# Kernel tuning notes

Measured on AMD Instinct MI355X. Metric: run time of the kernel, lower is better.

Reference implementation:

```python
import jax, jax.numpy as jnp
import numpy as np

N, E = 50000, 800000
F_IN, H, C = 128, 4, 32
NEG_SLOPE = 0.2

def setup_inputs() -> dict:
    key = jax.random.key(0)
    k1, k2, k3, k4, k5, k6 = jax.random.split(key, 6)
    x = jax.random.normal(k1, (N, F_IN), dtype=jnp.float32)
    edge_index = jax.random.randint(k2, (2, E), 0, N, dtype=jnp.int64)
    # GATConv params: lin weight [F_IN, H*C], att_src/att_dst [H, C], bias [H*C]
    W = jax.random.normal(k3, (F_IN, H * C), dtype=jnp.float32) * (1.0 / np.sqrt(F_IN))
    att_src = jax.random.normal(k4, (H, C), dtype=jnp.float32) * (1.0 / np.sqrt(C))
    att_dst = jax.random.normal(k5, (H, C), dtype=jnp.float32) * (1.0 / np.sqrt(C))
    bias = jax.random.normal(k6, (H * C,), dtype=jnp.float32) * 0.01
    return {"x": x, "edge_index": edge_index, "W": W, "att_src": att_src, "att_dst": att_dst, "bias": bias}

def reference(x, edge_index, W, att_src, att_dst, bias):
    # Linear transform: [N, H, C]
    h = (x @ W).reshape(N, H, C)
    # Per-node attention logits: [N, H]
    a_src = jnp.einsum('nhc,hc->nh', h, att_src)
    a_dst = jnp.einsum('nhc,hc->nh', h, att_dst)
    # PyG GATConv adds self-loops by default
    loop = jnp.arange(N, dtype=edge_index.dtype)
    src = jnp.concatenate([edge_index[0], loop])  # message source j
    dst = jnp.concatenate([edge_index[1], loop])  # message target i
    # Edge logits + LeakyReLU: [E+N, H]
    e = jax.nn.leaky_relu(a_src[src] + a_dst[dst], NEG_SLOPE)
    # Segment softmax over incoming edges per target node
    m = jax.ops.segment_max(e, dst, num_segments=N)  # [N, H]
    e_exp = jnp.exp(e - m[dst])
    denom = jax.ops.segment_sum(e_exp, dst, num_segments=N)  # [N, H]
    att = e_exp / denom[dst]  # [E+N, H]
    # Scatter-add weighted messages: [N, H, C]
    out = jax.ops.segment_sum(h[src] * att[:, :, None], dst, num_segments=N)
    return out.reshape(N, H * C) + bias
```

## Files before the change

kernel.cpp:

```cpp
#include <hip/hip_runtime.h>
#include <cstdint>

#define NNODES 50000
#define NEDGES 800000
#define NEG 0.2f
#define NBKT 196
#define BCAP 5120
#define GEMM_BLOCKS 782

typedef __attribute__((ext_vector_type(8))) short short8;
typedef __attribute__((ext_vector_type(4))) float f32x4;

#define AS_STRIDE 136
#define CS_STRIDE 132

__device__ __forceinline__ float leaky(float v) { return v > 0.f ? v : NEG * v; }

__device__ __forceinline__ unsigned short f2bf(float f) {
    unsigned int u = __float_as_uint(f);
    u += 0x7fff + ((u >> 16) & 1);
    return (unsigned short)(u >> 16);
}

template <int NW>
__device__ __forceinline__ int block_excl_scan(int v, int t) {
    __shared__ int wsum[NW];
    const int lane = t & 63, wv = t >> 6;
    int x = v;
    #pragma unroll
    for (int m = 1; m < 64; m <<= 1) {
        int u = __shfl_up(x, m);
        if (lane >= m) x += u;
    }
    if (lane == 63) wsum[wv] = x;
    __syncthreads();
    if (t == 0) {
        int run = 0;
        #pragma unroll
        for (int i = 0; i < NW; ++i) { int tmp = wsum[i]; wsum[i] = run; run += tmp; }
    }
    __syncthreads();
    return x - v + wsum[wv];
}

__global__ __launch_bounds__(256) void wt_k(const float* __restrict__ W,
                                            const float* __restrict__ att_src,
                                            const float* __restrict__ att_dst,
                                            unsigned short* __restrict__ wt,
                                            uint4* __restrict__ battf,
                                            int* __restrict__ bcnt) {
    const int t = threadIdx.x;
    if (blockIdx.x < 16) {
        int i = blockIdx.x * 256 + t;
        int k = i >> 5, n4 = (i & 31) * 4;
        float4 wv = ((const float4*)W)[i];
        wt[(n4 + 0) * 128 + k] = f2bf(wv.x);
        wt[(n4 + 1) * 128 + k] = f2bf(wv.y);
        wt[(n4 + 2) * 128 + k] = f2bf(wv.z);
        wt[(n4 + 3) * 128 + k] = f2bf(wv.w);
        return;
    }
    __shared__ float wsd[2][128][4];
    if (t < NBKT) bcnt[t] = 0;
    const int k = t & 127, which = t >> 7;
    const float* av = which ? att_dst : att_src;
    #pragma unroll
    for (int h = 0; h < 4; ++h) {
        float s = 0.f;
        #pragma unroll
        for (int c4 = 0; c4 < 8; ++c4) {
            float4 wv = ((const float4*)(W + k * 128 + h * 32))[c4];
            float4 a  = ((const float4*)(av + h * 32))[c4];
            s += wv.x * a.x + wv.y * a.y + wv.z * a.z + wv.w * a.w;
        }
        wsd[which][k][h] = s;
    }
    __syncthreads();
    const int s = t >> 6, lane = t & 63;
    const int quad = lane >> 4, m16 = lane & 15;
    unsigned short fr[8];
    #pragma unroll
    for (int j = 0; j < 8; ++j) {
        int kk = s * 32 + quad * 8 + j;
        float v = 0.f;
        if (m16 < 4)      v = wsd[0][kk][m16];
        else if (m16 < 8) v = wsd[1][kk][m16 - 4];
        fr[j] = f2bf(v);
    }
    battf[s * 64 + lane] = make_uint4(
        ((unsigned)fr[1] << 16) | fr[0], ((unsigned)fr[3] << 16) | fr[2],
        ((unsigned)fr[5] << 16) | fr[4], ((unsigned)fr[7] << 16) | fr[6]);
}

__global__ __launch_bounds__(256) void fused_k(const float* __restrict__ x,
                                               const unsigned short* __restrict__ wt,
                                               const uint4* __restrict__ battf,
                                               unsigned short* __restrict__ hb,
                                               float* __restrict__ a_src,
                                               float* __restrict__ a_dst,
                                               const int* __restrict__ ei,
                                               int* __restrict__ bcnt,
                                               unsigned int* __restrict__ bktdata) {
    __shared__ __align__(16) char smem[52224];
    const int tid = threadIdx.x;

    if (blockIdx.x < GEMM_BLOCKS) {
        unsigned short* As = (unsigned short*)smem;
        unsigned short* Bs = (unsigned short*)(smem + 17408);
        float*          Cs = (float*)smem;
        const int rbase = blockIdx.x * 64;

        #pragma unroll
        for (int i = 0; i < 8; ++i) {
            int f = tid + i * 256;
            int r = f >> 5, c4 = (f & 31) * 4;
            float4 xv = make_float4(0.f, 0.f, 0.f, 0.f);
            if (rbase + r < NNODES) xv = ((const float4*)x)[(size_t)(rbase + r) * 32 + (f & 31)];
            unsigned int p0 = ((unsigned int)f2bf(xv.y) << 16) | f2bf(xv.x);
            unsigned int p1 = ((unsigned int)f2bf(xv.w) << 16) | f2bf(xv.z);
            *(uint2*)(As + r * AS_STRIDE + c4) = make_uint2(p0, p1);
        }
        #pragma unroll
        for (int i = 0; i < 8; ++i) {
            int c = tid + i * 256;
            int n = c >> 4, k8 = (c & 15) * 8;
            uint4 wv = ((const uint4*)wt)[c];
            *(uint4*)(Bs + n * AS_STRIDE + k8) = wv;
        }
        __syncthreads();

        const int lane = tid & 63, w = tid >> 6;
        const int quad = lane >> 4, m16 = lane & 15;

        short8 af[4];
        #pragma unroll
        for (int s = 0; s < 4; ++s)
            af[s] = *(const short8*)(As + (w * 16 + m16) * AS_STRIDE + s * 32 + quad * 8);

        f32x4 acc[8];
        #pragma unroll
        for (int t = 0; t < 8; ++t) acc[t] = (f32x4){0.f, 0.f, 0.f, 0.f};

        #pragma unroll
        for (int t = 0; t < 8; ++t) {
            #pragma unroll
            for (int s = 0; s < 4; ++s) {
                short8 bf = *(const short8*)(Bs + (t * 16 + m16) * AS_STRIDE + s * 32 + quad * 8);
                acc[t] = __builtin_amdgcn_mfma_f32_16x16x32_bf16(af[s], bf, acc[t], 0, 0, 0);
            }
        }

        f32x4 accL = (f32x4){0.f, 0.f, 0.f, 0.f};
        #pragma unroll
        for (int s = 0; s < 4; ++s) {
            uint4 bw = battf[s * 64 + lane];
            accL = __builtin_amdgcn_mfma_f32_16x16x32_bf16(af[s], *(short8*)&bw, accL, 0, 0, 0);
        }
        __syncthreads();

        #pragma unroll
        for (int t = 0; t < 8; ++t)
            #pragma unroll
            for (int r = 0; r < 4; ++r)
                Cs[(w * 16 + quad * 4 + r) * CS_STRIDE + t * 16 + m16] = acc[t][r];
        __syncthreads();

        const int cp = lane;
        #pragma unroll
        for (int r = 0; r < 16; ++r) {
            int row = w * 16 + r;
            int row_g = rbase + row;
            float2 cv = *(const float2*)(Cs + row * CS_STRIDE + 2 * cp);
            ushort2 hs;
            hs.x = f2bf(cv.x); hs.y = f2bf(cv.y);
            if (row_g < NNODES) ((ushort2*)(hb + (size_t)row_g * 128))[cp] = hs;
        }
        #pragma unroll
        for (int r = 0; r < 4; ++r) {
            int row_g = rbase + w * 16 + quad * 4 + r;
            if (row_g < NNODES) {
                if (m16 < 4)      a_src[row_g * 4 + m16]       = accL[r];
                else if (m16 < 8) a_dst[row_g * 4 + (m16 - 4)] = accL[r];
            }
        }
    } else {
        int* lhist = (int*)smem;
        int* lofs  = lhist + NBKT;
        int* lcur  = lofs + NBKT;
        int* gbase = lcur + NBKT;
        unsigned int* staged = (unsigned int*)(gbase + NBKT);
        const int b = blockIdx.x - GEMM_BLOCKS, t = tid;
        for (int i = t; i < NBKT; i += 256) lhist[i] = 0;
        __syncthreads();
        unsigned int pk[16];
        int bk[16];
        const int e0 = b * 4096;
        #pragma unroll
        for (int i = 0; i < 16; ++i) {
            int e = e0 + i * 256 + t;
            if (e < NEDGES) {
                int s = ei[e], d = ei[NEDGES + e];
                bk[i] = d >> 8;
                pk[i] = ((unsigned)bk[i] << 24) | ((unsigned)(d & 255) << 16) | (unsigned)s;
                atomicAdd(&lhist[bk[i]], 1);
            } else bk[i] = -1;
        }
        __syncthreads();
        int v = (t < NBKT) ? lhist[t] : 0;
        int excl = block_excl_scan<4>(v, t);
        if (t < NBKT) { lofs[t] = excl; lcur[t] = excl; }
        __syncthreads();
        if (t < NBKT) gbase[t] = (v > 0) ? atomicAdd(&bcnt[t], v) : 0;
        #pragma unroll
        for (int i = 0; i < 16; ++i) {
            if (bk[i] >= 0) {
                int pos = atomicAdd(&lcur[bk[i]], 1);
                staged[pos] = pk[i];
            }
        }
        __syncthreads();
        const int total = lofs[NBKT - 1] + lhist[NBKT - 1];
        for (int i = t; i < total; i += 256) {
            unsigned int ent = staged[i];
            int bb = ent >> 24;
            int pos = gbase[bb] + (i - lofs[bb]);
            bktdata[(size_t)bb * BCAP + pos] = ent & 0x00FFFFFFu;
        }
    }
}

__global__ __launch_bounds__(512) void sort_k(const int* __restrict__ bcnt,
                                              const unsigned int* __restrict__ bktdata,
                                              int* __restrict__ off,
                                              int* __restrict__ csr) {
    __shared__ unsigned int staged[BCAP];
    __shared__ int lcnt[256];
    __shared__ int lcur[256];
    __shared__ int sbase, scnt;
    const int b = blockIdx.x, t = threadIdx.x;
    int bv = (t < NBKT) ? bcnt[t] : 0;
    int bexcl = block_excl_scan<8>(bv, t);
    if (t == b) { sbase = bexcl; scnt = bv; }
    if (t < 256) lcnt[t] = 0;
    __syncthreads();
    const int cnt = scnt, base = sbase;
    for (int i = t; i < cnt; i += 512) staged[i] = bktdata[(size_t)b * BCAP + i];
    __syncthreads();
    for (int i = t; i < cnt; i += 512) atomicAdd(&lcnt[(staged[i] >> 16) & 0xFF], 1);
    __syncthreads();
    int v = (t < 256) ? lcnt[t] : 0;
    int excl = block_excl_scan<8>(v, t);
    if (t < 256) {
        lcur[t] = excl;
        const int node = b * 256 + t;
        if (node <= NNODES) off[node] = base + excl;
    }
    __syncthreads();
    for (int i = t; i < cnt; i += 512) {
        unsigned int ent = staged[i];
        int pos = atomicAdd(&lcur[(ent >> 16) & 0xFF], 1);
        csr[base + pos] = (int)(ent & 0xFFFFu);
    }
}

__global__ __launch_bounds__(256) void gather_k(const int* __restrict__ off,
                                                const int* __restrict__ csr,
                                                const unsigned short* __restrict__ hb,
                                                const float* __restrict__ a_src,
                                                const float* __restrict__ a_dst,
                                                const float* __restrict__ bias,
                                                float* __restrict__ out) {
    const int wid = threadIdx.x >> 6, lane = threadIdx.x & 63;
    const int n = blockIdx.x * 4 + wid;
    if (n >= NNODES) return;
    const int head = lane >> 4;
    const int sub  = lane & 15;
    const int g = head, q = sub;
    const int head_c = q >> 2;

    const float a_d = a_dst[n * 4 + head];
    float acc[8];
    #pragma unroll
    for (int k = 0; k < 8; ++k) acc[k] = 0.f;

    if (g == 0) {
        float wsc = __expf(leaky(a_src[n * 4 + head_c] + a_dst[n * 4 + head_c]));
        uint4 hv = ((const uint4*)(hb + (size_t)n * 128))[q];
        acc[0] = wsc * __uint_as_float(hv.x << 16);
        acc[1] = wsc * __uint_as_float(hv.x & 0xffff0000u);
        acc[2] = wsc * __uint_as_float(hv.y << 16);
        acc[3] = wsc * __uint_as_float(hv.y & 0xffff0000u);
        acc[4] = wsc * __uint_as_float(hv.z << 16);
        acc[5] = wsc * __uint_as_float(hv.z & 0xffff0000u);
        acc[6] = wsc * __uint_as_float(hv.w << 16);
        acc[7] = wsc * __uint_as_float(hv.w & 0xffff0000u);
    }
    float denom = (sub == 0) ? __expf(leaky(a_src[n * 4 + head] + a_d)) : 0.f;

    const int beg = off[n], end = off[n + 1];
    for (int base = beg; base < end; base += 16) {
        int m = end - base; if (m > 16) m = 16;
        int s = 0;
        float w = 0.f;
        if (sub < m) {
            s = csr[base + sub];
            w = __expf(leaky(a_src[s * 4 + head] + a_d));
        }
        denom += w;
        #pragma unroll
        for (int jj = 0; jj < 4; ++jj) {
            int j = jj * 4 + g;
            int   sj = __shfl(s, j);
            float wj = __shfl(w, (head_c << 4) | j);
            if (j < m) {
                uint4 hv = ((const uint4*)(hb + (size_t)sj * 128))[q];
                acc[0] += wj * __uint_as_float(hv.x << 16);
                acc[1] += wj * __uint_as_float(hv.x & 0xffff0000u);
                acc[2] += wj * __uint_as_float(hv.y << 16);
                acc[3] += wj * __uint_as_float(hv.y & 0xffff0000u);
                acc[4] += wj * __uint_as_float(hv.z << 16);
                acc[5] += wj * __uint_as_float(hv.z & 0xffff0000u);
                acc[6] += wj * __uint_as_float(hv.w << 16);
                acc[7] += wj * __uint_as_float(hv.w & 0xffff0000u);
            }
        }
    }
    #pragma unroll
    for (int mm = 8; mm >= 1; mm >>= 1) denom += __shfl_xor(denom, mm, 16);
    const float inv = __frcp_rn(__shfl(denom, head_c << 4));
    #pragma unroll
    for (int k = 0; k < 8; ++k) {
        acc[k] += __shfl_xor(acc[k], 16);
        acc[k] += __shfl_xor(acc[k], 32);
    }
    if (g == 0) {
        float4 b0 = ((const float4*)bias)[2 * q];
        float4 b1 = ((const float4*)bias)[2 * q + 1];
        float4* orow = (float4*)(out + (size_t)n * 128);
        orow[2 * q]     = make_float4(acc[0] * inv + b0.x, acc[1] * inv + b0.y,
                                      acc[2] * inv + b0.z, acc[3] * inv + b0.w);
        orow[2 * q + 1] = make_float4(acc[4] * inv + b1.x, acc[5] * inv + b1.y,
                                      acc[6] * inv + b1.z, acc[7] * inv + b1.w);
    }
}

extern "C" void kernel_launch(void* const* d_in, const int* in_sizes, int n_in,
                              void* d_out, int out_size, void* d_ws, size_t ws_size,
                              hipStream_t stream) {
    const float* x     = (const float*)d_in[0];
    const int*   ei    = (const int*)d_in[1];
    const float* W     = (const float*)d_in[2];
    const float* att_s = (const float*)d_in[3];
    const float* att_d = (const float*)d_in[4];
    const float* bias  = (const float*)d_in[5];
    float*       out   = (float*)d_out;
    char*        ws    = (char*)d_ws;

    unsigned short* hb = (unsigned short*)(ws);
    float* a_src  = (float*)(ws + 12800000);
    float* a_dst  = (float*)(ws + 13600000);
    int*   off    = (int*)  (ws + 14400000);
    int*   csr    = (int*)  (ws + 14600768);
    unsigned int* bktdata = (unsigned int*)(ws + 17800768);
    int*   bcnt   = (int*)  (ws + 21814848);
    unsigned short* wt = (unsigned short*)(ws + 21815632);
    uint4* battf  = (uint4*)(ws + 21848400);

    wt_k    <<<17, 256, 0, stream>>>(W, att_s, att_d, wt, battf, bcnt);
    fused_k <<<GEMM_BLOCKS + NBKT, 256, 0, stream>>>(x, wt, battf, hb,
                                                     a_src, a_dst, ei, bcnt, bktdata);
    sort_k  <<<NBKT, 512, 0, stream>>>(bcnt, bktdata, off, csr);
    gather_k<<<12500, 256, 0, stream>>>(off, csr, hb, a_src, a_dst, bias, out);
}
```

Baseline: 157.0 us.

## Precompute edge attention weights and softmax denominators in sort kernel

Moves the per-edge exp(leaky) weight computation and the per-node denominator sum out of the gather kernel into the CSR sort kernel. Edge weights are written to a float4 buffer aligned with the CSR, and the reciprocal denominators and self-loop weights are written per node. The gather kernel then reads precomputed weights instead of gathering a_src per edge and reducing the denominator with shuffles. In exchange it adds about 12.8MB of extra writes and reads plus shared-memory float atomics in the sort kernel, which has only 196 blocks.

```diff
diff --git a/kernel.cpp b/kernel.cpp
--- a/kernel.cpp
+++ b/kernel.cpp
@@ -231,17 +231,41 @@
 
 __global__ __launch_bounds__(512) void sort_k(const int* __restrict__ bcnt,
                                               const unsigned int* __restrict__ bktdata,
+                                              const float* __restrict__ a_src,
+                                              const float* __restrict__ a_dst,
                                               int* __restrict__ off,
-                                              int* __restrict__ csr) {
+                                              int* __restrict__ csr,
+                                              float4* __restrict__ wbuf,
+                                              float4* __restrict__ dinvb,
+                                              float4* __restrict__ wselfb) {
     __shared__ unsigned int staged[BCAP];
     __shared__ int lcnt[256];
     __shared__ int lcur[256];
+    __shared__ float adl[256][4];
+    __shared__ float dsum[256][4];
     __shared__ int sbase, scnt;
     const int b = blockIdx.x, t = threadIdx.x;
     int bv = (t < NBKT) ? bcnt[t] : 0;
     int bexcl = block_excl_scan<8>(bv, t);
     if (t == b) { sbase = bexcl; scnt = bv; }
-    if (t < 256) lcnt[t] = 0;
+    if (t < 256) {
+        lcnt[t] = 0;
+        const int nd = b * 256 + t;
+        if (nd < NNODES) {
+            float4 as = ((const float4*)a_src)[nd];
+            float4 ad = ((const float4*)a_dst)[nd];
+            adl[t][0] = ad.x; adl[t][1] = ad.y; adl[t][2] = ad.z; adl[t][3] = ad.w;
+            float w0 = __expf(leaky(as.x + ad.x));
+            float w1 = __expf(leaky(as.y + ad.y));
+            float w2 = __expf(leaky(as.z + ad.z));
+            float w3 = __expf(leaky(as.w + ad.w));
+            dsum[t][0] = w0; dsum[t][1] = w1; dsum[t][2] = w2; dsum[t][3] = w3;
+            wselfb[nd] = make_float4(w0, w1, w2, w3);
+        } else {
+            adl[t][0] = adl[t][1] = adl[t][2] = adl[t][3] = 0.f;
+            dsum[t][0] = dsum[t][1] = dsum[t][2] = dsum[t][3] = 1.f;
+        }
+    }
     __syncthreads();
     const int cnt = scnt, base = sbase;
     for (int i = t; i < cnt; i += 512) staged[i] = bktdata[(size_t)b * BCAP + i];
@@ -258,33 +282,51 @@
     __syncthreads();
     for (int i = t; i < cnt; i += 512) {
         unsigned int ent = staged[i];
-        int pos = atomicAdd(&lcur[(ent >> 16) & 0xFF], 1);
-        csr[base + pos] = (int)(ent & 0xFFFFu);
+        int loc = (ent >> 16) & 0xFF;
+        int s = (int)(ent & 0xFFFFu);
+        int pos = atomicAdd(&lcur[loc], 1);
+        csr[base + pos] = s;
+        float4 as = ((const float4*)a_src)[s];
+        float w0 = __expf(leaky(as.x + adl[loc][0]));
+        float w1 = __expf(leaky(as.y + adl[loc][1]));
+        float w2 = __expf(leaky(as.z + adl[loc][2]));
+        float w3 = __expf(leaky(as.w + adl[loc][3]));
+        wbuf[base + pos] = make_float4(w0, w1, w2, w3);
+        atomicAdd(&dsum[loc][0], w0);
+        atomicAdd(&dsum[loc][1], w1);
+        atomicAdd(&dsum[loc][2], w2);
+        atomicAdd(&dsum[loc][3], w3);
+    }
+    __syncthreads();
+    if (t < 256) {
+        const int nd = b * 256 + t;
+        if (nd < NNODES)
+            dinvb[nd] = make_float4(__frcp_rn(dsum[t][0]), __frcp_rn(dsum[t][1]),
+                                    __frcp_rn(dsum[t][2]), __frcp_rn(dsum[t][3]));
     }
 }
 
 __global__ __launch_bounds__(256) void gather_k(const int* __restrict__ off,
                                                 const int* __restrict__ csr,
                                                 const unsigned short* __restrict__ hb,
-                                                const float* __restrict__ a_src,
-                                                const float* __restrict__ a_dst,
+                                                const float* __restrict__ wbuf,
+                                                const float* __restrict__ dinvb,
+                                                const float* __restrict__ wselfb,
                                                 const float* __restrict__ bias,
                                                 float* __restrict__ out) {
     const int wid = threadIdx.x >> 6, lane = threadIdx.x & 63;
     const int n = blockIdx.x * 4 + wid;
     if (n >= NNODES) return;
-    const int head = lane >> 4;
-    const int sub  = lane & 15;
-    const int g = head, q = sub;
+    const int g = lane >> 4;
+    const int q = lane & 15;
     const int head_c = q >> 2;
 
-    const float a_d = a_dst[n * 4 + head];
     float acc[8];
     #pragma unroll
     for (int k = 0; k < 8; ++k) acc[k] = 0.f;
 
     if (g == 0) {
-        float wsc = __expf(leaky(a_src[n * 4 + head_c] + a_dst[n * 4 + head_c]));
+        float wsc = wselfb[n * 4 + head_c];
         uint4 hv = ((const uint4*)(hb + (size_t)n * 128))[q];
         acc[0] = wsc * __uint_as_float(hv.x << 16);
         acc[1] = wsc * __uint_as_float(hv.x & 0xffff0000u);
@@ -295,24 +337,16 @@
         acc[6] = wsc * __uint_as_float(hv.w << 16);
         acc[7] = wsc * __uint_as_float(hv.w & 0xffff0000u);
     }
-    float denom = (sub == 0) ? __expf(leaky(a_src[n * 4 + head] + a_d)) : 0.f;
 
     const int beg = off[n], end = off[n + 1];
     for (int base = beg; base < end; base += 16) {
         int m = end - base; if (m > 16) m = 16;
-        int s = 0;
-        float w = 0.f;
-        if (sub < m) {
-            s = csr[base + sub];
-            w = __expf(leaky(a_src[s * 4 + head] + a_d));
-        }
-        denom += w;
         #pragma unroll
         for (int jj = 0; jj < 4; ++jj) {
             int j = jj * 4 + g;
-            int   sj = __shfl(s, j);
-            float wj = __shfl(w, (head_c << 4) | j);
             if (j < m) {
+                int   sj = csr[base + j];
+                float wj = wbuf[(base + j) * 4 + head_c];
                 uint4 hv = ((const uint4*)(hb + (size_t)sj * 128))[q];
                 acc[0] += wj * __uint_as_float(hv.x << 16);
                 acc[1] += wj * __uint_as_float(hv.x & 0xffff0000u);
@@ -326,14 +360,12 @@
         }
     }
     #pragma unroll
-    for (int mm = 8; mm >= 1; mm >>= 1) denom += __shfl_xor(denom, mm, 16);
-    const float inv = __frcp_rn(__shfl(denom, head_c << 4));
-    #pragma unroll
     for (int k = 0; k < 8; ++k) {
         acc[k] += __shfl_xor(acc[k], 16);
         acc[k] += __shfl_xor(acc[k], 32);
     }
     if (g == 0) {
+        const float inv = dinvb[n * 4 + head_c];
         float4 b0 = ((const float4*)bias)[2 * q];
         float4 b1 = ((const float4*)bias)[2 * q + 1];
         float4* orow = (float4*)(out + (size_t)n * 128);
@@ -365,10 +397,16 @@
     int*   bcnt   = (int*)  (ws + 21814848);
     unsigned short* wt = (unsigned short*)(ws + 21815632);
     uint4* battf  = (uint4*)(ws + 21848400);
+    float4* wbuf  = (float4*)(ws + 21852496);
+    float4* dinvb = (float4*)(ws + 34652496);
+    float4* wselfb= (float4*)(ws + 35452496);
 
     wt_k    <<<17, 256, 0, stream>>>(W, att_s, att_d, wt, battf, bcnt);
     fused_k <<<GEMM_BLOCKS + NBKT, 256, 0, stream>>>(x, wt, battf, hb,
                                                      a_src, a_dst, ei, bcnt, bktdata);
-    sort_k  <<<NBKT, 512, 0, stream>>>(bcnt, bktdata, off, csr);
-    gather_k<<<12500, 256, 0, stream>>>(off, csr, hb, a_src, a_dst, bias, out);
-}
+    sort_k  <<<NBKT, 512, 0, stream>>>(bcnt, bktdata, a_src, a_dst, off, csr,
+                                       wbuf, dinvb, wselfb);
+    gather_k<<<12500, 256, 0, stream>>>(off, csr, hb, (const float*)wbuf,
+                                        (const float*)dinvb, (const float*)wselfb,
+                                        bias, out);
+}
```

New measurement: 175.4 us. +11.7%, slower.
